# Optimization experiments

Hardware: AMD Instinct MI355X
Metric: run time of the kernel (lower is better)

Reference implementation:

```python
import jax, jax.numpy as jnp
import numpy as np

N_NODES = 131072
N_DST = 16384        # batch_size * num_supernodes = 8 * 2048
DEG = 16
N_EDGES = N_DST * DEG
IN_DIM, HID, NDIM = 3, 256, 2
POS_STD = 1.0


def _linear_params(key, fan_in, fan_out):
    # xavier_uniform weights, zero bias; torch Linear stores W as [out, in]
    limit = np.sqrt(6.0 / (fan_in + fan_out)).astype(np.float32)
    w = jax.random.uniform(key, (fan_out, fan_in), jnp.float32, -limit, limit)
    return w, jnp.zeros((fan_out,), jnp.float32)


def setup_inputs() -> dict:
    key = jax.random.key(0)
    ks = jax.random.split(key, 12)
    x = jax.random.normal(ks[0], (N_NODES, IN_DIM), jnp.float32)
    mesh_pos = jax.random.uniform(ks[1], (N_NODES, NDIM), jnp.float32)
    # dst column sorted, each supernode id 0..N_DST-1 appears DEG times (segment_csr layout)
    dst = jnp.repeat(jnp.arange(N_DST, dtype=jnp.int64), DEG)
    src = jax.random.randint(ks[2], (N_EDGES,), 0, N_NODES, jnp.int64)
    mesh_edges = jnp.stack([dst, src], axis=1)  # [E, 2] = (dst, src)
    batch_idx = jnp.repeat(jnp.arange(8, dtype=jnp.int64), N_NODES // 8)
    ip_w1, ip_b1 = _linear_params(ks[3], IN_DIM, HID)
    ip_w2, ip_b2 = _linear_params(ks[4], HID, HID)
    ip_w3, ip_b3 = _linear_params(ks[5], HID, HID)
    msg_w1, msg_b1 = _linear_params(ks[6], 2 * HID, 2 * HID)
    msg_w2, msg_b2 = _linear_params(ks[7], 2 * HID, HID)
    msg_w3, msg_b3 = _linear_params(ks[8], HID, HID)
    b_fourier = jax.random.normal(ks[9], (HID // 2, NDIM), jnp.float32) * POS_STD
    return {
        "x": x, "mesh_pos": mesh_pos, "mesh_edges": mesh_edges, "batch_idx": batch_idx,
        "ip_w1": ip_w1, "ip_b1": ip_b1, "ip_w2": ip_w2, "ip_b2": ip_b2,
        "ip_w3": ip_w3, "ip_b3": ip_b3, "b_fourier": b_fourier,
        "msg_w1": msg_w1, "msg_b1": msg_b1, "msg_w2": msg_w2, "msg_b2": msg_b2,
        "msg_w3": msg_w3, "msg_b3": msg_b3,
        "batch_size": 8, "num_supernodes": 2048,
    }


def reference(x, mesh_pos, mesh_edges, batch_idx,
              ip_w1, ip_b1, ip_w2, ip_b2, ip_w3, ip_b3, b_fourier,
              msg_w1, msg_b1, msg_w2, msg_b2, msg_w3, msg_b3,
              batch_size, num_supernodes):
    gelu = lambda t: jax.nn.gelu(t, approximate=False)  # torch nn.GELU default (erf)
    # input_proj MLP
    h = gelu(x @ ip_w1.T + ip_b1)
    h = gelu(h @ ip_w2.T + ip_b2)
    h = h @ ip_w3.T + ip_b3
    # gaussian sincos positional embedding
    proj = (2.0 * jnp.pi) * (mesh_pos @ b_fourier.T)  # [N, HID/2]
    h = h + jnp.concatenate([jnp.cos(proj), jnp.sin(proj)], axis=-1)
    # edge gather + concat + message MLP
    dst, src = mesh_edges[:, 0], mesh_edges[:, 1]
    m = jnp.concatenate([h[src], h[dst]], axis=1)  # [E, 2*HID]
    m = gelu(m @ msg_w1.T + msg_b1)
    m = gelu(m @ msg_w2.T + msg_b2)
    m = m @ msg_w3.T + msg_b3
    # segment mean over (sorted, compact) destination supernodes
    num_dst = batch_size * num_supernodes
    sums = jax.ops.segment_sum(m, dst, num_segments=num_dst)
    counts = jax.ops.segment_sum(jnp.ones((dst.shape[0],), m.dtype), dst, num_segments=num_dst)
    out = sums / jnp.maximum(counts, 1.0)[:, None]
    return out.reshape(batch_size, num_supernodes, out.shape[-1])
```

## Files before the change

kernel.cpp:

```cpp
#include <hip/hip_runtime.h>
#include <math.h>

#define N_NODES 131072
#define N_DST   16384
#define DEG     16
#define HID     256
#define N_EDGES 262144

typedef __bf16 bf16_8 __attribute__((ext_vector_type(8)));
typedef float  f32_4  __attribute__((ext_vector_type(4)));

__device__ __forceinline__ float gelu_f(float v) {
    float u = fmaf(v * v, -0.10294324f, -2.30220819f) * v;
    float e;
    asm("v_exp_f32 %0, %1" : "=v"(e) : "v"(u));
    return v * __builtin_amdgcn_rcpf(1.0f + e);
}
__device__ __forceinline__ f32_4 zero4() {
    f32_4 z; z[0] = 0.f; z[1] = 0.f; z[2] = 0.f; z[3] = 0.f; return z;
}

__device__ __forceinline__ void load_lds16(const __bf16* g, __bf16* l) {
    __builtin_amdgcn_global_load_lds(
        (__attribute__((address_space(1))) void*)g,
        (__attribute__((address_space(3))) void*)l, 16, 0, 0);
}

__global__ void prep_kernel(__bf16* __restrict__ out,
                            const float* __restrict__ w2,
                            const float* __restrict__ w3,
                            const float* __restrict__ mw1,
                            const float* __restrict__ mw2,
                            const float* __restrict__ mw3) {
    int stride = gridDim.x * blockDim.x;
    for (int i = blockIdx.x * blockDim.x + threadIdx.x; i < 589824; i += stride) {
        float v;
        if      (i <  65536) v = w2[i];
        else if (i < 131072) v = w3[i - 65536];
        else if (i < 393216) v = mw1[i - 131072];
        else if (i < 524288) v = mw2[i - 393216];
        else                 v = mw3[i - 524288];
        out[i] = (__bf16)v;
    }
}

__global__ __launch_bounds__(256) void enc1_kernel(
    const float* __restrict__ x, const float* __restrict__ w1,
    const float* __restrict__ b1, __bf16* __restrict__ h1) {
    const int c8   = threadIdx.x & 31;
    const int nloc = threadIdx.x >> 5;
    float w[24], bb[8];
    #pragma unroll
    for (int i = 0; i < 6; i++) *(float4*)&w[i * 4] = ((const float4*)w1)[c8 * 6 + i];
    *(float4*)&bb[0] = ((const float4*)b1)[c8 * 2 + 0];
    *(float4*)&bb[4] = ((const float4*)b1)[c8 * 2 + 1];
    for (int n = blockIdx.x * 8 + nloc; n < N_NODES; n += gridDim.x * 8) {
        float x0 = x[n * 3 + 0], x1 = x[n * 3 + 1], x2 = x[n * 3 + 2];
        bf16_8 o;
        #pragma unroll
        for (int j = 0; j < 8; j++) {
            float v = fmaf(x2, w[j * 3 + 2],
                      fmaf(x1, w[j * 3 + 1],
                      fmaf(x0, w[j * 3 + 0], bb[j])));
            o[j] = (__bf16)gelu_f(v);
        }
        *(bf16_8*)&h1[(size_t)n * 256 + c8 * 8] = o;
    }
}

__global__ __launch_bounds__(256, 2) void enc23_kernel(
    __bf16* __restrict__ hA,
    const __bf16* __restrict__ W2, const float* __restrict__ b2,
    const __bf16* __restrict__ W3, const float* __restrict__ b3,
    const float* __restrict__ pos, const float* __restrict__ bfour)
{
    __shared__ __align__(16) __bf16 sA[64 * 64];
    __shared__ __align__(16) __bf16 sB[16384];
    __shared__ __align__(16) __bf16 sH2[64 * 256];

    const int tid = threadIdx.x;
    const int m0  = blockIdx.x * 64;
    const int wave = tid >> 6, lane = tid & 63, ln = lane & 15, quad = lane >> 4;
    const int wm = wave >> 1, wn = wave & 1;

    const __bf16* pA[2];
    #pragma unroll
    for (int i = 0; i < 2; i++) {
        int idx = i * 256 + tid;
        int row = idx >> 3, kg = (idx & 7) ^ (row & 7);
        pA[i] = hA + (size_t)(m0 + row) * 256 + kg * 8;
    }

    f32_4 acc[2][8];
    #pragma unroll
    for (int i = 0; i < 2; i++)
        #pragma unroll
        for (int j = 0; j < 8; j++) acc[i][j] = zero4();

    bf16_8 ar[2];
    #pragma unroll
    for (int i = 0; i < 2; i++) ar[i] = *(const bf16_8*)pA[i];

    #pragma unroll
    for (int kb = 0; kb < 4; kb++) {
        if (kb > 0) __syncthreads();
        #pragma unroll
        for (int i = 0; i < 2; i++)
            *(bf16_8*)&sA[(i * 256 + tid) * 8] = ar[i];
        #pragma unroll
        for (int i = 0; i < 8; i++) {
            int idx = i * 256 + tid;
            int row = idx >> 3, kg = (idx & 7) ^ (row & 7);
            load_lds16(W2 + (size_t)row * 256 + kb * 64 + kg * 8, &sB[idx * 8]);
        }
        __syncthreads();
        if (kb < 3) {
            #pragma unroll
            for (int i = 0; i < 2; i++)
                ar[i] = *(const bf16_8*)(pA[i] + (kb + 1) * 64);
        }
        #pragma unroll
        for (int ks = 0; ks < 2; ks++) {
            int c = ks * 4 + quad;
            bf16_8 af[2], bfr[8];
            #pragma unroll
            for (int mt = 0; mt < 2; mt++) {
                int mr = wm * 32 + mt * 16 + ln;
                af[mt] = *(const bf16_8*)&sA[mr * 64 + (c ^ (mr & 7)) * 8];
            }
            #pragma unroll
            for (int nt = 0; nt < 8; nt++) {
                int nr = wn * 128 + nt * 16 + ln;
                bfr[nt] = *(const bf16_8*)&sB[nr * 64 + (c ^ (nr & 7)) * 8];
            }
            #pragma unroll
            for (int mt = 0; mt < 2; mt++)
                #pragma unroll
                for (int nt = 0; nt < 8; nt++)
                    acc[mt][nt] = __builtin_amdgcn_mfma_f32_16x16x32_bf16(af[mt], bfr[nt], acc[mt][nt], 0, 0, 0);
        }
    }
    #pragma unroll
    for (int nt = 0; nt < 8; nt++) {
        int col = wn * 128 + nt * 16 + ln;
        float bb = b2[col];
        #pragma unroll
        for (int mt = 0; mt < 2; mt++) {
            #pragma unroll
            for (int r = 0; r < 4; r++) {
                int row = wm * 32 + mt * 16 + quad * 4 + r;
                sH2[row * 256 + ((col + row * 8) & 255)] = (__bf16)gelu_f(acc[mt][nt][r] + bb);
            }
        }
    }
    #pragma unroll
    for (int i = 0; i < 2; i++)
        #pragma unroll
        for (int j = 0; j < 8; j++) acc[i][j] = zero4();
    __syncthreads();

    #pragma unroll
    for (int kb = 0; kb < 4; kb++) {
        if (kb > 0) __syncthreads();
        #pragma unroll
        for (int i = 0; i < 8; i++) {
            int idx = i * 256 + tid;
            int row = idx >> 3, kg = (idx & 7) ^ (row & 7);
            load_lds16(W3 + (size_t)row * 256 + kb * 64 + kg * 8, &sB[idx * 8]);
        }
        __syncthreads();
        #pragma unroll
        for (int ks = 0; ks < 2; ks++) {
            int c = ks * 4 + quad;
            int k0 = kb * 64 + ks * 32 + quad * 8;
            bf16_8 af[2], bfr[8];
            #pragma unroll
            for (int mt = 0; mt < 2; mt++) {
                int mr = wm * 32 + mt * 16 + ln;
                af[mt] = *(const bf16_8*)&sH2[mr * 256 + ((k0 + mr * 8) & 255)];
            }
            #pragma unroll
            for (int nt = 0; nt < 8; nt++) {
                int nr = wn * 128 + nt * 16 + ln;
                bfr[nt] = *(const bf16_8*)&sB[nr * 64 + (c ^ (nr & 7)) * 8];
            }
            #pragma unroll
            for (int mt = 0; mt < 2; mt++)
                #pragma unroll
                for (int nt = 0; nt < 8; nt++)
                    acc[mt][nt] = __builtin_amdgcn_mfma_f32_16x16x32_bf16(af[mt], bfr[nt], acc[mt][nt], 0, 0, 0);
        }
    }
    __syncthreads();
    __bf16* buf = sB + wave * 4096;
    float b3r[8], Bc0[8], Bc1[8];
    #pragma unroll
    for (int nt = 0; nt < 8; nt++) {
        int col = wn * 128 + nt * 16 + ln;
        b3r[nt] = b3[col];
        int jm = col & 127;
        Bc0[nt] = bfour[jm * 2 + 0];
        Bc1[nt] = bfour[jm * 2 + 1];
    }
    const bool iscos = (wn == 0);
    #pragma unroll
    for (int mt = 0; mt < 2; mt++) {
        #pragma unroll
        for (int r = 0; r < 4; r++) {
            int rowL = mt * 16 + quad * 4 + r;
            int rowE = m0 + wm * 32 + rowL;
            float p0 = pos[rowE * 2 + 0], p1 = pos[rowE * 2 + 1];
            #pragma unroll
            for (int nt = 0; nt < 8; nt++) {
                float f = 6.2831853071795864f * fmaf(p1, Bc1[nt], p0 * Bc0[nt]);
                float v = acc[mt][nt][r] + b3r[nt] + (iscos ? __cosf(f) : __sinf(f));
                int colL = nt * 16 + ln;
                buf[rowL * 128 + ((colL + rowL * 8) & 127)] = (__bf16)v;
            }
        }
    }
    #pragma unroll
    for (int p = 0; p < 8; p++) {
        int rowL = p * 4 + (lane >> 4);
        int c8 = lane & 15;
        bf16_8 vv = *(const bf16_8*)&buf[rowL * 128 + ((c8 * 8 + rowL * 8) & 127)];
        *(bf16_8*)&hA[(size_t)(m0 + wm * 32 + rowL) * 256 + wn * 128 + c8 * 8] = vv;
    }
}

__global__ __launch_bounds__(512, 1) void msg_fused(
    const __bf16* __restrict__ h, const int* __restrict__ edges,
    const __bf16* __restrict__ W1a, const __bf16* __restrict__ dmat,
    const __bf16* __restrict__ W2, const float* __restrict__ b2,
    __bf16* __restrict__ p2)
{
    __shared__ __align__(16) __bf16 sH[32768];
    __shared__ __align__(16) __bf16 sB[2][16384];
    __shared__ __align__(16) __bf16 sM1[16384];

    const int tid = threadIdx.x;
    const int e0  = blockIdx.x * 128;
    const int wave = tid >> 6, lane = tid & 63, ln = lane & 15, quad = lane >> 4;
    const int wm = wave >> 1, wn = wave & 1;

    int* s_src = (int*)sM1;
    if (tid < 128) s_src[tid] = edges[2 * (e0 + tid) + 1];
    __syncthreads();

    auto stage_w1 = [&](int q, int kb, int p) {
        const __bf16* s0 = W1a + (size_t)(q * 128) * 512 + kb * 128;
        #pragma unroll
        for (int i = 0; i < 4; i++) {
            int idx = i * 512 + tid;
            int r = idx >> 4, kg = (idx & 15) ^ (r & 7);
            load_lds16(s0 + r * 512 + kg * 8, &sB[p][idx * 8]);
        }
    };
    auto stage_w2 = [&](int q, int kb2, int p) {
        const __bf16* s0 = W2 + q * 128 + kb2 * 64;
        #pragma unroll
        for (int i = 0; i < 4; i++) {
            int idx = i * 512 + tid;
            int r = idx >> 3, kg = (idx & 7) ^ (r & 7);
            load_lds16(s0 + (size_t)r * 512 + kg * 8, &sB[p][idx * 8]);
        }
    };

    #pragma unroll
    for (int i = 0; i < 8; i++) {
        int idx = i * 512 + tid;
        int row = idx >> 5, kg = (idx & 31) ^ (row & 7);
        load_lds16(h + (size_t)s_src[row] * 256 + kg * 8, &sH[idx * 8]);
    }
    stage_w1(0, 0, 0);
    __syncthreads();

    f32_4 acc2[2][8];
    #pragma unroll
    for (int i = 0; i < 2; i++)
        #pragma unroll
        for (int j = 0; j < 8; j++) acc2[i][j] = zero4();

    #pragma unroll 1
    for (int q = 0; q < 4; q++) {
        const int colbase = q * 128 + wn * 64;
        float bd[2][4];
        #pragma unroll
        for (int nt = 0; nt < 4; nt++) {
            #pragma unroll
            for (int mt = 0; mt < 2; mt++) {
                int gid = blockIdx.x * 8 + wm * 2 + mt;
                bd[mt][nt] = (float)dmat[(size_t)gid * 512 + colbase + nt * 16 + ln];
            }
        }
        f32_4 acc1[2][4];
        #pragma unroll
        for (int i = 0; i < 2; i++)
            #pragma unroll
            for (int j = 0; j < 4; j++) acc1[i][j] = zero4();

        stage_w1(q, 1, 1);
        #pragma unroll
        for (int ks = 0; ks < 4; ks++) {
            int c = ks * 4 + quad;
            bf16_8 af[2], bfr[4];
            #pragma unroll
            for (int mt = 0; mt < 2; mt++) {
                int mr = wm * 32 + mt * 16 + ln;
                af[mt] = *(const bf16_8*)&sH[mr * 256 + ((c ^ (mr & 7)) * 8)];
            }
            #pragma unroll
            for (int nt = 0; nt < 4; nt++) {
                int nr = wn * 64 + nt * 16 + ln;
                bfr[nt] = *(const bf16_8*)&sB[0][nr * 128 + ((c ^ (nr & 7)) * 8)];
            }
            #pragma unroll
            for (int mt = 0; mt < 2; mt++)
                #pragma unroll
                for (int nt = 0; nt < 4; nt++)
                    acc1[mt][nt] = __builtin_amdgcn_mfma_f32_16x16x32_bf16(af[mt], bfr[nt], acc1[mt][nt], 0, 0, 0);
        }
        __syncthreads();

        stage_w2(q, 0, 0);
        #pragma unroll
        for (int ks = 0; ks < 4; ks++) {
            int cb = ks * 4 + quad;
            int ca = 16 + cb;
            bf16_8 af[2], bfr[4];
            #pragma unroll
            for (int mt = 0; mt < 2; mt++) {
                int mr = wm * 32 + mt * 16 + ln;
                af[mt] = *(const bf16_8*)&sH[mr * 256 + ((ca ^ (mr & 7)) * 8)];
            }
            #pragma unroll
            for (int nt = 0; nt < 4; nt++) {
                int nr = wn * 64 + nt * 16 + ln;
                bfr[nt] = *(const bf16_8*)&sB[1][nr * 128 + ((cb ^ (nr & 7)) * 8)];
            }
            #pragma unroll
            for (int mt = 0; mt < 2; mt++)
                #pragma unroll
                for (int nt = 0; nt < 4; nt++)
                    acc1[mt][nt] = __builtin_amdgcn_mfma_f32_16x16x32_bf16(af[mt], bfr[nt], acc1[mt][nt], 0, 0, 0);
        }
        #pragma unroll
        for (int mt = 0; mt < 2; mt++) {
            #pragma unroll
            for (int nt = 0; nt < 4; nt++) {
                #pragma unroll
                for (int r = 0; r < 4; r++) {
                    int row = wm * 32 + mt * 16 + quad * 4 + r;
                    int colq = wn * 64 + nt * 16 + ln;
                    float v = gelu_f(acc1[mt][nt][r] + bd[mt][nt]);
                    sM1[row * 128 + ((colq + row * 8) & 127)] = (__bf16)v;
                }
            }
        }
        __syncthreads();

        stage_w2(q, 1, 1);
        #pragma unroll
        for (int ks = 0; ks < 2; ks++) {
            int k0 = ks * 32 + quad * 8;
            int cb2 = ks * 4 + quad;
            bf16_8 af[2], bfr[8];
            #pragma unroll
            for (int mt = 0; mt < 2; mt++) {
                int mr = wm * 32 + mt * 16 + ln;
                af[mt] = *(const bf16_8*)&sM1[mr * 128 + ((k0 + mr * 8) & 127)];
            }
            #pragma unroll
            for (int nt = 0; nt < 8; nt++) {
                int nr = wn * 128 + nt * 16 + ln;
                bfr[nt] = *(const bf16_8*)&sB[0][nr * 64 + ((cb2 ^ (nr & 7)) * 8)];
            }
            #pragma unroll
            for (int mt = 0; mt < 2; mt++)
                #pragma unroll
                for (int nt = 0; nt < 8; nt++)
                    acc2[mt][nt] = __builtin_amdgcn_mfma_f32_16x16x32_bf16(af[mt], bfr[nt], acc2[mt][nt], 0, 0, 0);
        }
        __syncthreads();

        if (q < 3) stage_w1(q + 1, 0, 0);
        #pragma unroll
        for (int ks = 0; ks < 2; ks++) {
            int k0 = 64 + ks * 32 + quad * 8;
            int cb2 = ks * 4 + quad;
            bf16_8 af[2], bfr[8];
            #pragma unroll
            for (int mt = 0; mt < 2; mt++) {
                int mr = wm * 32 + mt * 16 + ln;
                af[mt] = *(const bf16_8*)&sM1[mr * 128 + ((k0 + mr * 8) & 127)];
            }
            #pragma unroll
            for (int nt = 0; nt < 8; nt++) {
                int nr = wn * 128 + nt * 16 + ln;
                bfr[nt] = *(const bf16_8*)&sB[1][nr * 64 + ((cb2 ^ (nr & 7)) * 8)];
            }
            #pragma unroll
            for (int mt = 0; mt < 2; mt++)
                #pragma unroll
                for (int nt = 0; nt < 8; nt++)
                    acc2[mt][nt] = __builtin_amdgcn_mfma_f32_16x16x32_bf16(af[mt], bfr[nt], acc2[mt][nt], 0, 0, 0);
        }
        __syncthreads();
    }

    #pragma unroll
    for (int nt = 0; nt < 8; nt++) {
        int col = wn * 128 + nt * 16 + ln;
        float bb = b2[col];
        #pragma unroll
        for (int mt = 0; mt < 2; mt++) {
            float s = gelu_f(acc2[mt][nt][0] + bb) + gelu_f(acc2[mt][nt][1] + bb)
                    + gelu_f(acc2[mt][nt][2] + bb) + gelu_f(acc2[mt][nt][3] + bb);
            s += __shfl_xor(s, 16);
            s += __shfl_xor(s, 32);
            if (quad == 0) {
                int dstn = edges[2 * (e0 + (wm * 2 + mt) * 16)];
                p2[(size_t)dstn * HID + col] = (__bf16)(s * 0.0625f);
            }
        }
    }
}

template<int K, int GMODE, int WLD, int WOFF, bool BIAS, bool POOL_, bool F32OUT>
__global__ __launch_bounds__(256, 3) void mgemm(
    const __bf16* __restrict__ Ag, const __bf16* __restrict__ h,
    const int* __restrict__ edges, const __bf16* __restrict__ W,
    const float* __restrict__ bias, __bf16* __restrict__ Cb,
    float* __restrict__ Cf, int NB, int Nfull, int e0)
{
    __shared__ __align__(16) __bf16 sA[128 * 64];
    __shared__ __align__(16) __bf16 sB[128 * 64];
    __shared__ int s_idx[128];

    const int tid  = threadIdx.x;
    const int mblk = blockIdx.x / NB;
    const int nblk = blockIdx.x % NB;
    const int m0 = mblk * 128, n0 = nblk * 128;
    const int wave = tid >> 6, lane = tid & 63, ln = lane & 15, quad = lane >> 4;
    const int wm = wave >> 1, wn = wave & 1;

    if (GMODE) {
        if (tid < 128) {
            int r = m0 + tid;
            s_idx[tid] = (GMODE == 1) ? edges[2 * (e0 + r) + 1]
                                      : edges[2 * (DEG * r)];
        }
        __syncthreads();
    }

    const __bf16* pA[4];
    const __bf16* pB[4];
    #pragma unroll
    for (int i = 0; i < 4; i++) {
        int idx = i * 256 + tid;
        int row = idx >> 3, kg = (idx & 7) ^ (row & 7);
        pA[i] = GMODE ? h + (size_t)s_idx[row] * HID + kg * 8
                      : Ag + (size_t)(m0 + row) * K + kg * 8;
        pB[i] = W + (size_t)(n0 + row) * WLD + WOFF + kg * 8;
    }
    const int ach = quad ^ (ln & 7);
    const int aof[2] = { (wm * 64 + ln) * 64 + ach * 8, (wm * 64 + ln) * 64 + (ach ^ 4) * 8 };
    const int bof[2] = { (wn * 64 + ln) * 64 + ach * 8, (wn * 64 + ln) * 64 + (ach ^ 4) * 8 };

    f32_4 acc[4][4];
    #pragma unroll
    for (int i = 0; i < 4; i++)
        #pragma unroll
        for (int j = 0; j < 4; j++) acc[i][j] = zero4();

    bf16_8 ar[4], br[4];
    #pragma unroll
    for (int i = 0; i < 4; i++) {
        ar[i] = *(const bf16_8*)pA[i];
        br[i] = *(const bf16_8*)pB[i];
    }

    #pragma unroll
    for (int kb = 0; kb < K / 64; kb++) {
        if (kb > 0) __syncthreads();
        #pragma unroll
        for (int i = 0; i < 4; i++) {
            int idx = i * 256 + tid;
            *(bf16_8*)&sA[idx * 8] = ar[i];
            *(bf16_8*)&sB[idx * 8] = br[i];
        }
        __syncthreads();
        if (kb + 1 < K / 64) {
            #pragma unroll
            for (int i = 0; i < 4; i++) {
                ar[i] = *(const bf16_8*)(pA[i] + (kb + 1) * 64);
                br[i] = *(const bf16_8*)(pB[i] + (kb + 1) * 64);
            }
        }
        #pragma unroll
        for (int ks = 0; ks < 2; ks++) {
            bf16_8 af[4], bfr[4];
            #pragma unroll
            for (int mt = 0; mt < 4; mt++) af[mt]  = *(const bf16_8*)&sA[aof[ks] + mt * 1024];
            #pragma unroll
            for (int nt = 0; nt < 4; nt++) bfr[nt] = *(const bf16_8*)&sB[bof[ks] + nt * 1024];
            #pragma unroll
            for (int mt = 0; mt < 4; mt++)
                #pragma unroll
                for (int nt = 0; nt < 4; nt++)
                    acc[mt][nt] = __builtin_amdgcn_mfma_f32_16x16x32_bf16(af[mt], bfr[nt], acc[mt][nt], 0, 0, 0);
        }
    }

    if (POOL_) {
        #pragma unroll
        for (int nt = 0; nt < 4; nt++) {
            int col = n0 + wn * 64 + nt * 16 + ln;
            float bb = BIAS ? bias[col] : 0.f;
            #pragma unroll
            for (int mt = 0; mt < 4; mt++) {
                float s = gelu_f(acc[mt][nt][0] + bb) + gelu_f(acc[mt][nt][1] + bb)
                        + gelu_f(acc[mt][nt][2] + bb) + gelu_f(acc[mt][nt][3] + bb);
                s += __shfl_xor(s, 16);
                s += __shfl_xor(s, 32);
                if (quad == 0) {
                    int eg  = e0 + m0 + wm * 64 + mt * 16;
                    int dstn = edges[2 * eg];
                    Cb[(size_t)dstn * HID + col] = (__bf16)(s * 0.0625f);
                }
            }
        }
    } else if (F32OUT) {
        #pragma unroll
        for (int nt = 0; nt < 4; nt++) {
            int col = n0 + wn * 64 + nt * 16 + ln;
            float bb = BIAS ? bias[col] : 0.f;
            #pragma unroll
            for (int mt = 0; mt < 4; mt++) {
                #pragma unroll
                for (int r = 0; r < 4; r++) {
                    int rowE = m0 + wm * 64 + mt * 16 + quad * 4 + r;
                    Cf[(size_t)rowE * Nfull + col] = acc[mt][nt][r] + bb;
                }
            }
        }
    } else {
        __syncthreads();
        __bf16* sw = ((wave & 2) ? sB : sA) + (wave & 1) * 4096;
        #pragma unroll
        for (int nt = 0; nt < 4; nt++) {
            float bb = BIAS ? bias[n0 + wn * 64 + nt * 16 + ln] : 0.f;
            #pragma unroll
            for (int mt = 0; mt < 4; mt++) {
                #pragma unroll
                for (int r = 0; r < 4; r++) {
                    int rowL = mt * 16 + quad * 4 + r;
                    int colL = nt * 16 + ln;
                    sw[rowL * 64 + ((colL + rowL * 8) & 63)] = (__bf16)(acc[mt][nt][r] + bb);
                }
            }
        }
        __syncthreads();
        #pragma unroll
        for (int p = 0; p < 8; p++) {
            int rowL = p * 8 + (lane >> 3);
            int c8 = lane & 7;
            bf16_8 vv = *(const bf16_8*)&sw[rowL * 64 + ((c8 * 8 + rowL * 8) & 63)];
            int rowE = m0 + wm * 64 + rowL;
            *(bf16_8*)&Cb[(size_t)rowE * Nfull + n0 + wn * 64 + c8 * 8] = vv;
        }
    }
}

extern "C" void kernel_launch(void* const* d_in, const int* in_sizes, int n_in,
                              void* d_out, int out_size, void* d_ws, size_t ws_size,
                              hipStream_t stream) {
    const float* x     = (const float*)d_in[0];
    const float* pos   = (const float*)d_in[1];
    const int*   edges = (const int*)d_in[2];
    const float* ip_w1 = (const float*)d_in[4];
    const float* ip_b1 = (const float*)d_in[5];
    const float* ip_w2 = (const float*)d_in[6];
    const float* ip_b2 = (const float*)d_in[7];
    const float* ip_w3 = (const float*)d_in[8];
    const float* ip_b3 = (const float*)d_in[9];
    const float* bfour = (const float*)d_in[10];
    const float* mw1   = (const float*)d_in[11];
    const float* mb1   = (const float*)d_in[12];
    const float* mw2   = (const float*)d_in[13];
    const float* mb2   = (const float*)d_in[14];
    const float* mw3   = (const float*)d_in[15];
    const float* mb3   = (const float*)d_in[16];

    char* ws = (char*)d_ws;
    __bf16* hA = (__bf16*)ws;
    size_t off = (size_t)N_NODES * HID * 2;
    __bf16* wb = (__bf16*)(ws + off);
    off += (size_t)589824 * 2;
    off = (off + 255) & ~(size_t)255;
    __bf16* dbuf = (__bf16*)(ws + off);
    off += (size_t)N_DST * 512 * 2;
    __bf16* p2 = (__bf16*)(ws + off);
    off += (size_t)N_DST * HID * 2;

    __bf16* w2b  = wb;
    __bf16* w3b  = wb + 65536;
    __bf16* mw1b = wb + 131072;
    __bf16* mw2b = wb + 393216;
    __bf16* mw3b = wb + 524288;

    prep_kernel<<<2304, 256, 0, stream>>>(wb, ip_w2, ip_w3, mw1, mw2, mw3);

    enc1_kernel<<<2048, 256, 0, stream>>>(x, ip_w1, ip_b1, hA);
    enc23_kernel<<<2048, 256, 0, stream>>>(hA, w2b, ip_b2, w3b, ip_b3, pos, bfour);

    mgemm<256, 2, 512, 256, true, false, false><<<512, 256, 0, stream>>>(
        nullptr, hA, edges, mw1b, mb1, dbuf, nullptr, 4, 512, 0);

    msg_fused<<<2048, 512, 0, stream>>>(hA, edges, mw1b, dbuf, mw2b, mb2, p2);

    mgemm<256, 0, 256, 0, true, false, true><<<256, 256, 0, stream>>>(
        p2, nullptr, nullptr, mw3b, mb3, nullptr, (float*)d_out, 2, 256, 0);
}
```

Measured before the change: 419.9 us.

## Fuse first encoder layer into enc23 kernel and raise MFMA wave priority

Computes the first input-projection layer (3->256 with GELU) directly into shared memory inside the encoder GEMM kernel, so the 64MB bf16 intermediate is never written to or read back from global memory and one launch disappears. Weight staging for W3 is moved to overlap with the layer-2 epilogue, and the prep kernel becomes a one-element-per-thread grid. MFMA blocks in the message kernel are wrapped in s_setprio to favour matrix issue over other waves. Shared memory use drops (sA removed), but the layer-1 compute now sits on the GEMM kernel's critical path.

```diff
diff --git a/kernel.cpp b/kernel.cpp
--- a/kernel.cpp
+++ b/kernel.cpp
@@ -32,93 +32,76 @@
                             const float* __restrict__ mw1,
                             const float* __restrict__ mw2,
                             const float* __restrict__ mw3) {
-    int stride = gridDim.x * blockDim.x;
-    for (int i = blockIdx.x * blockDim.x + threadIdx.x; i < 589824; i += stride) {
-        float v;
-        if      (i <  65536) v = w2[i];
-        else if (i < 131072) v = w3[i - 65536];
-        else if (i < 393216) v = mw1[i - 131072];
-        else if (i < 524288) v = mw2[i - 393216];
-        else                 v = mw3[i - 524288];
-        out[i] = (__bf16)v;
-    }
-}
-
-__global__ __launch_bounds__(256) void enc1_kernel(
-    const float* __restrict__ x, const float* __restrict__ w1,
-    const float* __restrict__ b1, __bf16* __restrict__ h1) {
-    const int c8   = threadIdx.x & 31;
-    const int nloc = threadIdx.x >> 5;
-    float w[24], bb[8];
-    #pragma unroll
-    for (int i = 0; i < 6; i++) *(float4*)&w[i * 4] = ((const float4*)w1)[c8 * 6 + i];
-    *(float4*)&bb[0] = ((const float4*)b1)[c8 * 2 + 0];
-    *(float4*)&bb[4] = ((const float4*)b1)[c8 * 2 + 1];
-    for (int n = blockIdx.x * 8 + nloc; n < N_NODES; n += gridDim.x * 8) {
-        float x0 = x[n * 3 + 0], x1 = x[n * 3 + 1], x2 = x[n * 3 + 2];
-        bf16_8 o;
-        #pragma unroll
-        for (int j = 0; j < 8; j++) {
-            float v = fmaf(x2, w[j * 3 + 2],
-                      fmaf(x1, w[j * 3 + 1],
-                      fmaf(x0, w[j * 3 + 0], bb[j])));
-            o[j] = (__bf16)gelu_f(v);
-        }
-        *(bf16_8*)&h1[(size_t)n * 256 + c8 * 8] = o;
-    }
-}
-
-__global__ __launch_bounds__(256, 2) void enc23_kernel(
-    __bf16* __restrict__ hA,
+    int i = blockIdx.x * 256 + threadIdx.x;
+    if (i >= 589824) return;
+    float v;
+    if      (i <  65536) v = w2[i];
+    else if (i < 131072) v = w3[i - 65536];
+    else if (i < 393216) v = mw1[i - 131072];
+    else if (i < 524288) v = mw2[i - 393216];
+    else                 v = mw3[i - 524288];
+    out[i] = (__bf16)v;
+}
+
+__global__ __launch_bounds__(256, 2) void enc123_kernel(
+    const float* __restrict__ x, const float* __restrict__ ew1,
+    const float* __restrict__ eb1, __bf16* __restrict__ hA,
     const __bf16* __restrict__ W2, const float* __restrict__ b2,
     const __bf16* __restrict__ W3, const float* __restrict__ b3,
     const float* __restrict__ pos, const float* __restrict__ bfour)
 {
-    __shared__ __align__(16) __bf16 sA[64 * 64];
+    __shared__ __align__(16) __bf16 sH[64 * 256];
     __shared__ __align__(16) __bf16 sB[16384];
-    __shared__ __align__(16) __bf16 sH2[64 * 256];
 
     const int tid = threadIdx.x;
     const int m0  = blockIdx.x * 64;
     const int wave = tid >> 6, lane = tid & 63, ln = lane & 15, quad = lane >> 4;
     const int wm = wave >> 1, wn = wave & 1;
 
-    const __bf16* pA[2];
-    #pragma unroll
-    for (int i = 0; i < 2; i++) {
-        int idx = i * 256 + tid;
-        int row = idx >> 3, kg = (idx & 7) ^ (row & 7);
-        pA[i] = hA + (size_t)(m0 + row) * 256 + kg * 8;
-    }
-
-    f32_4 acc[2][8];
-    #pragma unroll
-    for (int i = 0; i < 2; i++)
-        #pragma unroll
-        for (int j = 0; j < 8; j++) acc[i][j] = zero4();
-
-    bf16_8 ar[2];
-    #pragma unroll
-    for (int i = 0; i < 2; i++) ar[i] = *(const bf16_8*)pA[i];
-
-    #pragma unroll
-    for (int kb = 0; kb < 4; kb++) {
-        if (kb > 0) __syncthreads();
-        #pragma unroll
-        for (int i = 0; i < 2; i++)
-            *(bf16_8*)&sA[(i * 256 + tid) * 8] = ar[i];
+    auto stage_w = [&](const __bf16* W, int kb) {
         #pragma unroll
         for (int i = 0; i < 8; i++) {
             int idx = i * 256 + tid;
             int row = idx >> 3, kg = (idx & 7) ^ (row & 7);
-            load_lds16(W2 + (size_t)row * 256 + kb * 64 + kg * 8, &sB[idx * 8]);
-        }
-        __syncthreads();
-        if (kb < 3) {
-            #pragma unroll
-            for (int i = 0; i < 2; i++)
-                ar[i] = *(const bf16_8*)(pA[i] + (kb + 1) * 64);
-        }
+            load_lds16(W + (size_t)row * 256 + kb * 64 + kg * 8, &sB[idx * 8]);
+        }
+    };
+
+    stage_w(W2, 0);
+    {
+        const int c8 = tid & 31;
+        const int rl = tid >> 5;
+        float w[24], bb[8];
+        #pragma unroll
+        for (int i = 0; i < 6; i++) *(float4*)&w[i * 4] = ((const float4*)ew1)[c8 * 6 + i];
+        *(float4*)&bb[0] = ((const float4*)eb1)[c8 * 2 + 0];
+        *(float4*)&bb[4] = ((const float4*)eb1)[c8 * 2 + 1];
+        #pragma unroll
+        for (int rr = 0; rr < 8; rr++) {
+            int row = rr * 8 + rl;
+            int g = m0 + row;
+            float x0 = x[g * 3 + 0], x1 = x[g * 3 + 1], x2 = x[g * 3 + 2];
+            bf16_8 o;
+            #pragma unroll
+            for (int j = 0; j < 8; j++) {
+                float v = fmaf(x2, w[j * 3 + 2],
+                          fmaf(x1, w[j * 3 + 1],
+                          fmaf(x0, w[j * 3 + 0], bb[j])));
+                o[j] = (__bf16)gelu_f(v);
+            }
+            *(bf16_8*)&sH[row * 256 + ((c8 ^ (row & 7)) * 8)] = o;
+        }
+    }
+    __syncthreads();
+
+    f32_4 acc[2][8];
+    #pragma unroll
+    for (int i = 0; i < 2; i++)
+        #pragma unroll
+        for (int j = 0; j < 8; j++) acc[i][j] = zero4();
+
+    #pragma unroll
+    for (int kb = 0; kb < 4; kb++) {
         #pragma unroll
         for (int ks = 0; ks < 2; ks++) {
             int c = ks * 4 + quad;
@@ -126,12 +109,12 @@
             #pragma unroll
             for (int mt = 0; mt < 2; mt++) {
                 int mr = wm * 32 + mt * 16 + ln;
-                af[mt] = *(const bf16_8*)&sA[mr * 64 + (c ^ (mr & 7)) * 8];
+                af[mt] = *(const bf16_8*)&sH[mr * 256 + ((kb * 8 + (c ^ (mr & 7))) * 8)];
             }
             #pragma unroll
             for (int nt = 0; nt < 8; nt++) {
                 int nr = wn * 128 + nt * 16 + ln;
-                bfr[nt] = *(const bf16_8*)&sB[nr * 64 + (c ^ (nr & 7)) * 8];
+                bfr[nt] = *(const bf16_8*)&sB[nr * 64 + ((c ^ (nr & 7)) * 8)];
             }
             #pragma unroll
             for (int mt = 0; mt < 2; mt++)
@@ -139,7 +122,13 @@
                 for (int nt = 0; nt < 8; nt++)
                     acc[mt][nt] = __builtin_amdgcn_mfma_f32_16x16x32_bf16(af[mt], bfr[nt], acc[mt][nt], 0, 0, 0);
         }
-    }
+        __syncthreads();
+        if (kb < 3) {
+            stage_w(W2, kb + 1);
+            __syncthreads();
+        }
+    }
+    stage_w(W3, 0);
     #pragma unroll
     for (int nt = 0; nt < 8; nt++) {
         int col = wn * 128 + nt * 16 + ln;
@@ -149,7 +138,7 @@
             #pragma unroll
             for (int r = 0; r < 4; r++) {
                 int row = wm * 32 + mt * 16 + quad * 4 + r;
-                sH2[row * 256 + ((col + row * 8) & 255)] = (__bf16)gelu_f(acc[mt][nt][r] + bb);
+                sH[row * 256 + ((col + row * 8) & 255)] = (__bf16)gelu_f(acc[mt][nt][r] + bb);
             }
         }
     }
@@ -161,14 +150,6 @@
 
     #pragma unroll
     for (int kb = 0; kb < 4; kb++) {
-        if (kb > 0) __syncthreads();
-        #pragma unroll
-        for (int i = 0; i < 8; i++) {
-            int idx = i * 256 + tid;
-            int row = idx >> 3, kg = (idx & 7) ^ (row & 7);
-            load_lds16(W3 + (size_t)row * 256 + kb * 64 + kg * 8, &sB[idx * 8]);
-        }
-        __syncthreads();
         #pragma unroll
         for (int ks = 0; ks < 2; ks++) {
             int c = ks * 4 + quad;
@@ -177,12 +158,12 @@
             #pragma unroll
             for (int mt = 0; mt < 2; mt++) {
                 int mr = wm * 32 + mt * 16 + ln;
-                af[mt] = *(const bf16_8*)&sH2[mr * 256 + ((k0 + mr * 8) & 255)];
+                af[mt] = *(const bf16_8*)&sH[mr * 256 + ((k0 + mr * 8) & 255)];
             }
             #pragma unroll
             for (int nt = 0; nt < 8; nt++) {
                 int nr = wn * 128 + nt * 16 + ln;
-                bfr[nt] = *(const bf16_8*)&sB[nr * 64 + (c ^ (nr & 7)) * 8];
+                bfr[nt] = *(const bf16_8*)&sB[nr * 64 + ((c ^ (nr & 7)) * 8)];
             }
             #pragma unroll
             for (int mt = 0; mt < 2; mt++)
@@ -190,8 +171,12 @@
                 for (int nt = 0; nt < 8; nt++)
                     acc[mt][nt] = __builtin_amdgcn_mfma_f32_16x16x32_bf16(af[mt], bfr[nt], acc[mt][nt], 0, 0, 0);
         }
-    }
-    __syncthreads();
+        __syncthreads();
+        if (kb < 3) {
+            stage_w(W3, kb + 1);
+            __syncthreads();
+        }
+    }
     __bf16* buf = sB + wave * 4096;
     float b3r[8], Bc0[8], Bc1[8];
     #pragma unroll
@@ -314,11 +299,13 @@
                 int nr = wn * 64 + nt * 16 + ln;
                 bfr[nt] = *(const bf16_8*)&sB[0][nr * 128 + ((c ^ (nr & 7)) * 8)];
             }
+            __builtin_amdgcn_s_setprio(1);
             #pragma unroll
             for (int mt = 0; mt < 2; mt++)
                 #pragma unroll
                 for (int nt = 0; nt < 4; nt++)
                     acc1[mt][nt] = __builtin_amdgcn_mfma_f32_16x16x32_bf16(af[mt], bfr[nt], acc1[mt][nt], 0, 0, 0);
+            __builtin_amdgcn_s_setprio(0);
         }
         __syncthreads();
 
@@ -338,11 +325,13 @@
                 int nr = wn * 64 + nt * 16 + ln;
                 bfr[nt] = *(const bf16_8*)&sB[1][nr * 128 + ((cb ^ (nr & 7)) * 8)];
             }
+            __builtin_amdgcn_s_setprio(1);
             #pragma unroll
             for (int mt = 0; mt < 2; mt++)
                 #pragma unroll
                 for (int nt = 0; nt < 4; nt++)
                     acc1[mt][nt] = __builtin_amdgcn_mfma_f32_16x16x32_bf16(af[mt], bfr[nt], acc1[mt][nt], 0, 0, 0);
+            __builtin_amdgcn_s_setprio(0);
         }
         #pragma unroll
         for (int mt = 0; mt < 2; mt++) {
@@ -375,11 +364,13 @@
                 int nr = wn * 128 + nt * 16 + ln;
                 bfr[nt] = *(const bf16_8*)&sB[0][nr * 64 + ((cb2 ^ (nr & 7)) * 8)];
             }
+            __builtin_amdgcn_s_setprio(1);
             #pragma unroll
             for (int mt = 0; mt < 2; mt++)
                 #pragma unroll
                 for (int nt = 0; nt < 8; nt++)
                     acc2[mt][nt] = __builtin_amdgcn_mfma_f32_16x16x32_bf16(af[mt], bfr[nt], acc2[mt][nt], 0, 0, 0);
+            __builtin_amdgcn_s_setprio(0);
         }
         __syncthreads();
 
@@ -399,11 +390,13 @@
                 int nr = wn * 128 + nt * 16 + ln;
                 bfr[nt] = *(const bf16_8*)&sB[1][nr * 64 + ((cb2 ^ (nr & 7)) * 8)];
             }
+            __builtin_amdgcn_s_setprio(1);
             #pragma unroll
             for (int mt = 0; mt < 2; mt++)
                 #pragma unroll
                 for (int nt = 0; nt < 8; nt++)
                     acc2[mt][nt] = __builtin_amdgcn_mfma_f32_16x16x32_bf16(af[mt], bfr[nt], acc2[mt][nt], 0, 0, 0);
+            __builtin_amdgcn_s_setprio(0);
         }
         __syncthreads();
     }
@@ -611,8 +604,8 @@
 
     prep_kernel<<<2304, 256, 0, stream>>>(wb, ip_w2, ip_w3, mw1, mw2, mw3);
 
-    enc1_kernel<<<2048, 256, 0, stream>>>(x, ip_w1, ip_b1, hA);
-    enc23_kernel<<<2048, 256, 0, stream>>>(hA, w2b, ip_b2, w3b, ip_b3, pos, bfour);
+    enc123_kernel<<<2048, 256, 0, stream>>>(x, ip_w1, ip_b1, hA,
+                                            w2b, ip_b2, w3b, ip_b3, pos, bfour);
 
     mgemm<256, 2, 512, 256, true, false, false><<<512, 256, 0, stream>>>(
         nullptr, hA, edges, mw1b, mb1, dbuf, nullptr, 4, 512, 0);
```

New measurement: 404.3 us. 1.04x faster.
